# Performance work log

Measured on AMD Instinct MI355X. Metric: run time of the kernel, lower is better.

The kernel has to match this reference:

```python
import jax, jax.numpy as jnp
import numpy as np

N_NODES = 100000
N_EDGES = 1600000
N_FEAT = 128
HIDDEN = 128
OUT = 1
NUM_GRAPHS = 2048


def setup_inputs() -> dict:
    key = jax.random.key(0)
    ks = jax.random.split(key, 8)
    x = jax.random.normal(ks[0], (N_NODES, N_FEAT), dtype=jnp.float32)
    edge_index = jax.random.randint(ks[1], (2, N_EDGES), 0, N_NODES, dtype=jnp.int64)
    batch = jnp.sort(jax.random.randint(ks[2], (N_NODES,), 0, NUM_GRAPHS, dtype=jnp.int64))
    s = 1.0 / np.sqrt(N_FEAT)
    W1 = jax.random.normal(ks[3], (N_FEAT, HIDDEN), dtype=jnp.float32) * s
    b1 = jnp.zeros((HIDDEN,), dtype=jnp.float32)
    W2 = jax.random.normal(ks[4], (HIDDEN, HIDDEN), dtype=jnp.float32) * s
    b2 = jnp.zeros((HIDDEN,), dtype=jnp.float32)
    Wlin = jax.random.normal(ks[5], (HIDDEN, OUT), dtype=jnp.float32) * s
    blin = jnp.zeros((OUT,), dtype=jnp.float32)
    return {"x": x, "edge_index": edge_index, "batch": batch,
            "W1": W1, "b1": b1, "W2": W2, "b2": b2, "Wlin": Wlin, "blin": blin}


def gcn_conv(x, W, b, src, dst, n_nodes):
    # PyG GCNConv: x' = D^{-1/2} (A + I) D^{-1/2} (X W) + b, deg includes self-loop
    xw = x @ W  # [N, H]
    deg = jax.ops.segment_sum(jnp.ones(src.shape[0], xw.dtype), dst, num_segments=n_nodes) + 1.0
    dinv = jax.lax.rsqrt(deg)
    norm = dinv[src] * dinv[dst]  # [E]
    agg = jax.ops.segment_sum(xw[src] * norm[:, None], dst, num_segments=n_nodes)
    # self-loop contribution: norm = deg^{-1}
    return agg + xw * (1.0 / deg)[:, None] + b


def global_mean_pool(x, batch, num_graphs):
    sums = jax.ops.segment_sum(x, batch, num_segments=num_graphs)
    cnts = jax.ops.segment_sum(jnp.ones(x.shape[0], x.dtype), batch, num_segments=num_graphs)
    return sums / jnp.maximum(cnts, 1.0)[:, None]


def reference(x, edge_index, batch, W1, b1, W2, b2, Wlin, blin):
    src, dst = edge_index[0], edge_index[1]
    n = x.shape[0]
    h = gcn_conv(x, W1, b1, src, dst, n)
    h = jax.nn.relu(h)  # dropout is a no-op in eval mode
    h = gcn_conv(h, W2, b2, src, dst, n)
    g = global_mean_pool(h, batch, NUM_GRAPHS)  # [G, H]
    return g @ Wlin + blin
```

## Files before the change

kernel.cpp:

```cpp
#include <hip/hip_runtime.h>

#define N_NODES   100000
#define N_EDGES   1600000
#define NFEAT     128
#define NGRAPHS   2048
#define CBSHIFT   8
#define NCB       ((N_NODES + 255) / 256)
#define P1_EPB    8192
#define GEMM_BLOCKS 782
#define BH_BLOCKS   256
#define DP_BLOCKS 100
#define DP_NPB    ((N_NODES + DP_BLOCKS - 1) / DP_BLOCKS)
#define G1_BLOCKS 2048
#define ZCNT      (NGRAPHS + NCB + 64 + 512 + NCB)

typedef __attribute__((ext_vector_type(8))) short short8;
typedef __attribute__((ext_vector_type(4))) float f32x4;

__device__ __forceinline__ unsigned short f2bf(float f) {
    unsigned int u = __float_as_uint(f);
    u += 0x7FFFu + ((u >> 16) & 1u);
    return (unsigned short)(u >> 16);
}

__device__ __forceinline__ void acc8s(float* acc, uint4 v, float s) {
    acc[0] = fmaf(s, __uint_as_float(v.x << 16), acc[0]);
    acc[1] = fmaf(s, __uint_as_float(v.x & 0xFFFF0000u), acc[1]);
    acc[2] = fmaf(s, __uint_as_float(v.y << 16), acc[2]);
    acc[3] = fmaf(s, __uint_as_float(v.y & 0xFFFF0000u), acc[3]);
    acc[4] = fmaf(s, __uint_as_float(v.z << 16), acc[4]);
    acc[5] = fmaf(s, __uint_as_float(v.z & 0xFFFF0000u), acc[5]);
    acc[6] = fmaf(s, __uint_as_float(v.w << 16), acc[6]);
    acc[7] = fmaf(s, __uint_as_float(v.w & 0xFFFF0000u), acc[7]);
}

__global__ __launch_bounds__(256) void k_misc(const float* __restrict__ W1,
                                              unsigned short* __restrict__ WT1,
                                              const float* __restrict__ W2,
                                              const float* __restrict__ Wlin,
                                              const float* __restrict__ b2,
                                              const float* __restrict__ blin,
                                              float* __restrict__ w2l,
                                              int* __restrict__ zeros) {
    const int blk = blockIdx.x;
    const int t = threadIdx.x;
    if (blk < 16) {
        int base = blk * 1024 + t * 4;
        #pragma unroll
        for (int q = 0; q < 4; ++q) {
            int i = base + q;
            int n = i >> 7, k = i & 127;
            WT1[i] = f2bf(W1[k * 128 + n]);
        }
    } else if (blk == 16) {
        __shared__ float s[256];
        int i = t >> 1, half = t & 1;
        float ps = 0.f;
        for (int j = half * 64; j < half * 64 + 64; ++j)
            ps += W2[i * 128 + j] * Wlin[j];
        s[t] = ps;
        __syncthreads();
        if (!half) w2l[i] = s[t] + s[t + 1];
        __syncthreads();
        float pc = (t < 128) ? b2[t] * Wlin[t] : 0.f;
        s[t] = pc;
        __syncthreads();
        for (int off = 128; off > 0; off >>= 1) {
            if (t < off) s[t] += s[t + off];
            __syncthreads();
        }
        if (t == 0) w2l[128] = s[0] + blin[0];
    } else {
        int i = (blk - 17) * 256 + t;
        if (i < ZCNT) zeros[i] = 0;
    }
}

__global__ __launch_bounds__(256) void k_gemm_bhist(const float* __restrict__ X,
                                                    const unsigned short* __restrict__ WT,
                                                    unsigned short* __restrict__ C,
                                                    const int* __restrict__ dst,
                                                    int* __restrict__ bcount) {
    if (blockIdx.x >= GEMM_BLOCKS) {
        __shared__ int h[NCB];
        for (int i = threadIdx.x; i < NCB; i += 256) h[i] = 0;
        __syncthreads();
        int b = blockIdx.x - GEMM_BLOCKS;
        int stride = BH_BLOCKS * 256;
        for (int e = b * 256 + threadIdx.x; e < N_EDGES; e += stride)
            atomicAdd(&h[dst[e] >> CBSHIFT], 1);
        __syncthreads();
        for (int i = threadIdx.x; i < NCB; i += 256) {
            int v = h[i];
            if (v) atomicAdd(&bcount[i], v);
        }
        return;
    }
    const int tid  = threadIdx.x;
    const int R0   = blockIdx.x * 128;
    const int wv   = tid >> 6;
    const int lane = tid & 63;
    const int m16  = lane & 15;
    const int quad = lane >> 4;
    const int r0 = R0 + wv * 32 + m16;
    const int r1 = r0 + 16;
    const bool ok0 = r0 < N_NODES, ok1 = r1 < N_NODES;

    f32x4 acc[2][8] = {};
    #pragma unroll
    for (int ks = 0; ks < 4; ++ks) {
        const int k0 = ks * 32 + quad * 8;
        short8 a0 = {}, a1 = {};
        if (ok0) {
            float4 f0 = *(const float4*)(X + (size_t)r0 * NFEAT + k0);
            float4 f1 = *(const float4*)(X + (size_t)r0 * NFEAT + k0 + 4);
            a0[0] = (short)f2bf(f0.x); a0[1] = (short)f2bf(f0.y);
            a0[2] = (short)f2bf(f0.z); a0[3] = (short)f2bf(f0.w);
            a0[4] = (short)f2bf(f1.x); a0[5] = (short)f2bf(f1.y);
            a0[6] = (short)f2bf(f1.z); a0[7] = (short)f2bf(f1.w);
        }
        if (ok1) {
            float4 f0 = *(const float4*)(X + (size_t)r1 * NFEAT + k0);
            float4 f1 = *(const float4*)(X + (size_t)r1 * NFEAT + k0 + 4);
            a1[0] = (short)f2bf(f0.x); a1[1] = (short)f2bf(f0.y);
            a1[2] = (short)f2bf(f0.z); a1[3] = (short)f2bf(f0.w);
            a1[4] = (short)f2bf(f1.x); a1[5] = (short)f2bf(f1.y);
            a1[6] = (short)f2bf(f1.z); a1[7] = (short)f2bf(f1.w);
        }
        #pragma unroll
        for (int ct = 0; ct < 8; ++ct) {
            short8 bb = *(const short8*)(WT + (ct * 16 + m16) * 128 + k0);
            acc[0][ct] = __builtin_amdgcn_mfma_f32_16x16x32_bf16(a0, bb, acc[0][ct], 0, 0, 0);
            acc[1][ct] = __builtin_amdgcn_mfma_f32_16x16x32_bf16(a1, bb, acc[1][ct], 0, 0, 0);
        }
    }
    #pragma unroll
    for (int t2 = 0; t2 < 2; ++t2) {
        int rbase = R0 + wv * 32 + t2 * 16 + quad * 4;
        #pragma unroll
        for (int reg = 0; reg < 4; ++reg) {
            int gr = rbase + reg;
            if (gr < N_NODES) {
                #pragma unroll
                for (int ct = 0; ct < 8; ++ct)
                    C[(size_t)gr * NFEAT + ct * 16 + m16] = f2bf(acc[t2][ct][reg]);
            }
        }
    }
}

__global__ __launch_bounds__(256) void k_p1(const int* __restrict__ src,
                                            const int* __restrict__ dst,
                                            const int* __restrict__ bcount,
                                            int* __restrict__ bstart,
                                            int* __restrict__ alloc,
                                            unsigned int* __restrict__ pairs) {
    __shared__ int hist[NCB], base[NCB], cur[NCB], bst[NCB], s[256];
    const int t = threadIdx.x;
    for (int i = t; i < NCB; i += 256) { hist[i] = 0; cur[i] = 0; }
    int v0 = (2 * t < NCB) ? bcount[2 * t] : 0;
    int v1 = (2 * t + 1 < NCB) ? bcount[2 * t + 1] : 0;
    int local = v0 + v1;
    s[t] = local;
    __syncthreads();
    for (int off = 1; off < 256; off <<= 1) {
        int x = (t >= off) ? s[t - off] : 0;
        __syncthreads();
        s[t] += x;
        __syncthreads();
    }
    int excl = s[t] - local;
    if (2 * t < NCB)     bst[2 * t] = excl;
    if (2 * t + 1 < NCB) bst[2 * t + 1] = excl + v0;
    if (blockIdx.x == 0) {
        if (2 * t < NCB)     bstart[2 * t] = excl;
        if (2 * t + 1 < NCB) bstart[2 * t + 1] = excl + v0;
        if (t == 255) bstart[NCB] = s[255];
    }
    __syncthreads();
    const int e0 = blockIdx.x * P1_EPB;
    const int e1 = min(e0 + P1_EPB, N_EDGES);
    for (int e = e0 + t; e < e1; e += 256)
        atomicAdd(&hist[dst[e] >> CBSHIFT], 1);
    __syncthreads();
    const int off0 = (blockIdx.x * 89) % NCB;
    for (int k = t; k < NCB; k += 256) {
        int i = k + off0;
        if (i >= NCB) i -= NCB;
        int c = hist[i];
        base[i] = c ? (bst[i] + atomicAdd(&alloc[i], c)) : 0;
    }
    __syncthreads();
    for (int e = e0 + t; e < e1; e += 256) {
        int d = dst[e];
        int b = d >> CBSHIFT;
        int r = atomicAdd(&cur[b], 1);
        pairs[base[b] + r] = (unsigned int)src[e] | ((unsigned int)(d & 255) << 17);
    }
}

__global__ __launch_bounds__(256) void k_p2(const unsigned int* __restrict__ pairs,
                                            const int* __restrict__ bstart,
                                            int* __restrict__ csr_src,
                                            int* __restrict__ row_start,
                                            int* __restrict__ indeg,
                                            float* __restrict__ dinv,
                                            int* __restrict__ dcount) {
    __shared__ int hist[256], sst[256], cur[256], s[256], dh[64];
    const int b = blockIdx.x;
    const int t = threadIdx.x;
    const int beg = bstart[b];
    const int end = bstart[b + 1];
    hist[t] = 0; cur[t] = 0;
    if (t < 64) dh[t] = 0;
    __syncthreads();
    for (int i = beg + t; i < end; i += 256)
        atomicAdd(&hist[pairs[i] >> 17], 1);
    __syncthreads();
    int v = hist[t];
    s[t] = v;
    __syncthreads();
    for (int off = 1; off < 256; off <<= 1) {
        int x = (t >= off) ? s[t - off] : 0;
        __syncthreads();
        s[t] += x;
        __syncthreads();
    }
    sst[t] = s[t] - v;
    __syncthreads();
    {
        int node = (b << CBSHIFT) + t;
        if (node < N_NODES) {
            row_start[node] = beg + sst[t];
            indeg[node] = v;
            dinv[node] = rsqrtf((float)v + 1.0f);
            atomicAdd(&dh[63 - min(v, 63)], 1);
        }
    }
    for (int i = beg + t; i < end; i += 256) {
        unsigned int pv = pairs[i];
        int dl = pv >> 17;
        int r = atomicAdd(&cur[dl], 1);
        csr_src[beg + sst[dl] + r] = (int)(pv & 0x1FFFFu);
    }
    __syncthreads();
    if (t < 64 && dh[t]) atomicAdd(&dcount[((b & 7) << 6) + t], dh[t]);
}

__global__ __launch_bounds__(256) void k_dperm(const int* __restrict__ indeg,
                                               const int* __restrict__ dcount,
                                               int* __restrict__ dalloc,
                                               int* __restrict__ perm) {
    __shared__ int h[64], base[64], cur[64], s[64];
    const int t = threadIdx.x;
    int v = 0;
    if (t < 64) {
        h[t] = 0; cur[t] = 0;
        #pragma unroll
        for (int sh = 0; sh < 8; ++sh) v += dcount[(sh << 6) + t];
        s[t] = v;
    }
    __syncthreads();
    for (int off = 1; off < 64; off <<= 1) {
        int x = (t >= off && t < 64) ? s[t - off] : 0;
        __syncthreads();
        if (t < 64) s[t] += x;
        __syncthreads();
    }
    int myst = (t < 64) ? s[t] - v : 0;
    const int i0 = blockIdx.x * DP_NPB;
    const int i1 = min(i0 + DP_NPB, N_NODES);
    for (int i = i0 + t; i < i1; i += 256)
        atomicAdd(&h[63 - min(indeg[i], 63)], 1);
    __syncthreads();
    if (t < 64) {
        int c = h[t];
        base[t] = c ? (myst + atomicAdd(&dalloc[t], c)) : 0;
    }
    __syncthreads();
    for (int i = i0 + t; i < i1; i += 256) {
        int bin = 63 - min(indeg[i], 63);
        int r = atomicAdd(&cur[bin], 1);
        perm[base[bin] + r] = i;
    }
}

__global__ __launch_bounds__(256) void k_gather1(const unsigned short* __restrict__ xwb,
                                                 const int* __restrict__ csr_src,
                                                 const int* __restrict__ row_start,
                                                 const int* __restrict__ indeg,
                                                 const float* __restrict__ dinv,
                                                 const float* __restrict__ b,
                                                 const float* __restrict__ w2l,
                                                 const int* __restrict__ perm,
                                                 float* __restrict__ z) {
    const int lane  = threadIdx.x & 63;
    const int p     = lane & 15;
    const int gbase = lane & 48;
    const int ngroups = G1_BLOCKS * 16;
    int gid = blockIdx.x * 16 + (threadIdx.x >> 4);
    const uint4* tab = (const uint4*)xwb;
    float4 b0 = *(const float4*)(b + p * 8);
    float4 b1 = *(const float4*)(b + p * 8 + 4);
    float4 w0 = *(const float4*)(w2l + p * 8);
    float4 w1 = *(const float4*)(w2l + p * 8 + 4);

    for (int nidx = gid; nidx < N_NODES; nidx += ngroups) {
        int node = perm[nidx];
        const int beg = row_start[node];
        const int cnt = indeg[node];
        float dvn = dinv[node];
        float acc[8] = {};
        acc8s(acc, tab[(size_t)node * 16 + p], dvn);
        int j = 0;
        #pragma unroll 1
        for (; j + 8 <= cnt; j += 8) {
            int   my   = csr_src[beg + j + (p & 7)];
            float mydv = dinv[my];
            uint4 v[8];
            #pragma unroll
            for (int q = 0; q < 8; ++q) {
                int idx = __shfl(my, gbase + q);
                v[q] = tab[(size_t)idx * 16 + p];
            }
            #pragma unroll
            for (int q = 0; q < 8; ++q) {
                float sv = __shfl(mydv, gbase + q);
                acc8s(acc, v[q], sv);
            }
        }
        #pragma unroll 1
        for (; j < cnt; ++j) {
            int idx = csr_src[beg + j];
            float sv = dinv[idx];
            acc8s(acc, tab[(size_t)idx * 16 + p], sv);
        }
        float s = fmaxf(acc[0] * dvn + b0.x, 0.f) * w0.x
                + fmaxf(acc[1] * dvn + b0.y, 0.f) * w0.y
                + fmaxf(acc[2] * dvn + b0.z, 0.f) * w0.z
                + fmaxf(acc[3] * dvn + b0.w, 0.f) * w0.w
                + fmaxf(acc[4] * dvn + b1.x, 0.f) * w1.x
                + fmaxf(acc[5] * dvn + b1.y, 0.f) * w1.y
                + fmaxf(acc[6] * dvn + b1.z, 0.f) * w1.z
                + fmaxf(acc[7] * dvn + b1.w, 0.f) * w1.w;
        s += __shfl_xor(s, 1);
        s += __shfl_xor(s, 2);
        s += __shfl_xor(s, 4);
        s += __shfl_xor(s, 8);
        if (p == 0) z[node] = s * dvn;
    }
}

__global__ __launch_bounds__(256) void k_gather2s(const float* __restrict__ z,
                                                  const int* __restrict__ csr_src,
                                                  const int* __restrict__ row_start,
                                                  const int* __restrict__ indeg,
                                                  const float* __restrict__ dinv,
                                                  const int* __restrict__ perm,
                                                  const int* __restrict__ batch,
                                                  float* __restrict__ gsum) {
    int nidx = blockIdx.x * blockDim.x + threadIdx.x;
    if (nidx >= N_NODES) return;
    int node = perm[nidx];
    const int beg = row_start[node];
    const int cnt = indeg[node];
    float a = z[node];
    int j = 0;
    #pragma unroll 1
    for (; j + 4 <= cnt; j += 4) {
        int i0 = csr_src[beg + j + 0];
        int i1 = csr_src[beg + j + 1];
        int i2 = csr_src[beg + j + 2];
        int i3 = csr_src[beg + j + 3];
        a += z[i0] + z[i1] + z[i2] + z[i3];
    }
    #pragma unroll 1
    for (; j < cnt; ++j)
        a += z[csr_src[beg + j]];
    atomicAdd(&gsum[batch[node]], a * dinv[node]);
}

__global__ void k_final(const float* __restrict__ gsum, const int* __restrict__ batch,
                        const float* __restrict__ c2, float* __restrict__ out) {
    int g = blockIdx.x * blockDim.x + threadIdx.x;
    if (g >= NGRAPHS) return;
    int lo = 0, hi = N_NODES;
    while (lo < hi) { int m = (lo + hi) >> 1; if (batch[m] < g) lo = m + 1; else hi = m; }
    int lb = lo;
    lo = 0; hi = N_NODES;
    int g1 = g + 1;
    while (lo < hi) { int m = (lo + hi) >> 1; if (batch[m] < g1) lo = m + 1; else hi = m; }
    float cnt = (float)(lo - lb);
    out[g] = gsum[g] / fmaxf(cnt, 1.0f) + c2[0];
}

extern "C" void kernel_launch(void* const* d_in, const int* in_sizes, int n_in,
                              void* d_out, int out_size, void* d_ws, size_t ws_size,
                              hipStream_t stream) {
    const float* x    = (const float*)d_in[0];
    const int*   ei   = (const int*)d_in[1];
    const int*   bat  = (const int*)d_in[2];
    const float* W1   = (const float*)d_in[3];
    const float* b1   = (const float*)d_in[4];
    const float* W2   = (const float*)d_in[5];
    const float* b2   = (const float*)d_in[6];
    const float* Wlin = (const float*)d_in[7];
    const float* blin = (const float*)d_in[8];
    float* out = (float*)d_out;

    const int* src = ei;
    const int* dst = ei + N_EDGES;

    const size_t NF = (size_t)N_NODES * NFEAT;
    unsigned short* bufA = (unsigned short*)d_ws;
    float* z       = (float*)(bufA + NF);
    float* dinv    = z + N_NODES;
    int* row_start = (int*)(dinv + N_NODES);
    int* indeg     = row_start + N_NODES;
    int* perm      = indeg + N_NODES;
    int* bstart    = perm + N_NODES;
    float* gsum    = (float*)(bstart + NCB + 1);
    int* alloc     = (int*)(gsum + NGRAPHS);
    int* dalloc    = alloc + NCB;
    int* dcount    = dalloc + 64;
    int* bcount    = dcount + 512;
    unsigned short* WT1 = (unsigned short*)(bcount + NCB);
    float* w2l     = (float*)(WT1 + 128 * 128);
    unsigned int* pairs = (unsigned int*)(w2l + 132);
    int* csr_src   = (int*)(pairs + N_EDGES);

    const int BS = 256;
    int p1_blocks   = (N_EDGES + P1_EPB - 1) / P1_EPB;
    int node_blocks = (N_NODES + BS - 1) / BS;
    int misc_blocks = 17 + (ZCNT + BS - 1) / BS;

    k_misc<<<misc_blocks, BS, 0, stream>>>(W1, WT1, W2, Wlin, b2, blin, w2l, (int*)gsum);
    k_gemm_bhist<<<GEMM_BLOCKS + BH_BLOCKS, BS, 0, stream>>>(x, WT1, bufA, dst, bcount);

    k_p1<<<p1_blocks, BS, 0, stream>>>(src, dst, bcount, bstart, alloc, pairs);
    k_p2<<<NCB, BS, 0, stream>>>(pairs, bstart, csr_src, row_start, indeg, dinv, dcount);
    k_dperm<<<DP_BLOCKS, BS, 0, stream>>>(indeg, dcount, dalloc, perm);

    k_gather1<<<G1_BLOCKS, BS, 0, stream>>>(bufA, csr_src, row_start, indeg, dinv, b1, w2l,
                                            perm, z);

    k_gather2s<<<node_blocks, BS, 0, stream>>>(z, csr_src, row_start, indeg, dinv, perm,
                                               bat, gsum);

    k_final<<<(NGRAPHS + BS - 1) / BS, BS, 0, stream>>>(gsum, bat, w2l + 128, out);
}
```

Before: 284.7 us.

## Fuse misc prep into GEMM kernel and fold final pooling into gather2

Removes the separate misc kernel. Each GEMM block now transposes and converts W1 to bf16 itself in shared memory, and the W2·Wlin and per-graph inverse-count work runs as extra blocks of the GEMM launch. The final kernel is folded into gather2 with a last-block-done counter, and zeroing now uses hipMemsetAsync. This cuts two kernel launches and their serialization gaps, at the cost of each GEMM block redoing the W1 conversion and a global atomic counter plus fence in gather2.

```diff
diff --git a/kernel.cpp b/kernel.cpp
--- a/kernel.cpp
+++ b/kernel.cpp
@@ -9,10 +9,12 @@
 #define P1_EPB    8192
 #define GEMM_BLOCKS 782
 #define BH_BLOCKS   256
+#define GC_BLOCKS   8
 #define DP_BLOCKS 100
 #define DP_NPB    ((N_NODES + DP_BLOCKS - 1) / DP_BLOCKS)
 #define G1_BLOCKS 2048
-#define ZCNT      (NGRAPHS + NCB + 64 + 512 + NCB)
+#define G2_BLOCKS ((N_NODES + 255) / 256)
+#define ZCNT      (NGRAPHS + NCB + 64 + 512 + NCB + 1)
 
 typedef __attribute__((ext_vector_type(8))) short short8;
 typedef __attribute__((ext_vector_type(4))) float f32x4;
@@ -34,72 +36,87 @@
     acc[7] = fmaf(s, __uint_as_float(v.w & 0xFFFF0000u), acc[7]);
 }
 
-__global__ __launch_bounds__(256) void k_misc(const float* __restrict__ W1,
-                                              unsigned short* __restrict__ WT1,
-                                              const float* __restrict__ W2,
-                                              const float* __restrict__ Wlin,
-                                              const float* __restrict__ b2,
-                                              const float* __restrict__ blin,
-                                              float* __restrict__ w2l,
-                                              int* __restrict__ zeros) {
+__global__ __launch_bounds__(256) void k_gemm_bhist(const float* __restrict__ X,
+                                                    const float* __restrict__ W1,
+                                                    unsigned short* __restrict__ C,
+                                                    const int* __restrict__ dst,
+                                                    int* __restrict__ bcount,
+                                                    const int* __restrict__ batch,
+                                                    float* __restrict__ invc,
+                                                    const float* __restrict__ W2,
+                                                    const float* __restrict__ Wlin,
+                                                    const float* __restrict__ b2,
+                                                    const float* __restrict__ blin,
+                                                    float* __restrict__ w2l) {
+    __shared__ unsigned short Ws[128][136];
     const int blk = blockIdx.x;
     const int t = threadIdx.x;
-    if (blk < 16) {
-        int base = blk * 1024 + t * 4;
-        #pragma unroll
-        for (int q = 0; q < 4; ++q) {
-            int i = base + q;
-            int n = i >> 7, k = i & 127;
-            WT1[i] = f2bf(W1[k * 128 + n]);
-        }
-    } else if (blk == 16) {
-        __shared__ float s[256];
+
+    if (blk >= GEMM_BLOCKS + BH_BLOCKS + GC_BLOCKS) {
+        __shared__ float fs[256];
         int i = t >> 1, half = t & 1;
         float ps = 0.f;
         for (int j = half * 64; j < half * 64 + 64; ++j)
             ps += W2[i * 128 + j] * Wlin[j];
-        s[t] = ps;
-        __syncthreads();
-        if (!half) w2l[i] = s[t] + s[t + 1];
+        fs[t] = ps;
+        __syncthreads();
+        if (!half) w2l[i] = fs[t] + fs[t + 1];
         __syncthreads();
         float pc = (t < 128) ? b2[t] * Wlin[t] : 0.f;
-        s[t] = pc;
+        fs[t] = pc;
         __syncthreads();
         for (int off = 128; off > 0; off >>= 1) {
-            if (t < off) s[t] += s[t + off];
+            if (t < off) fs[t] += fs[t + off];
             __syncthreads();
         }
-        if (t == 0) w2l[128] = s[0] + blin[0];
-    } else {
-        int i = (blk - 17) * 256 + t;
-        if (i < ZCNT) zeros[i] = 0;
-    }
-}
-
-__global__ __launch_bounds__(256) void k_gemm_bhist(const float* __restrict__ X,
-                                                    const unsigned short* __restrict__ WT,
-                                                    unsigned short* __restrict__ C,
-                                                    const int* __restrict__ dst,
-                                                    int* __restrict__ bcount) {
-    if (blockIdx.x >= GEMM_BLOCKS) {
-        __shared__ int h[NCB];
-        for (int i = threadIdx.x; i < NCB; i += 256) h[i] = 0;
-        __syncthreads();
-        int b = blockIdx.x - GEMM_BLOCKS;
+        if (t == 0) w2l[128] = fs[0] + blin[0];
+        return;
+    }
+    if (blk >= GEMM_BLOCKS + BH_BLOCKS) {
+        int g = (blk - GEMM_BLOCKS - BH_BLOCKS) * 256 + t;
+        if (g < NGRAPHS) {
+            int lo = 0, hi = N_NODES;
+            while (lo < hi) { int m = (lo + hi) >> 1; if (batch[m] < g) lo = m + 1; else hi = m; }
+            int lb = lo;
+            lo = 0; hi = N_NODES;
+            int g1 = g + 1;
+            while (lo < hi) { int m = (lo + hi) >> 1; if (batch[m] < g1) lo = m + 1; else hi = m; }
+            invc[g] = 1.0f / fmaxf((float)(lo - lb), 1.0f);
+        }
+        return;
+    }
+    if (blk >= GEMM_BLOCKS) {
+        int* h = (int*)&Ws[0][0];
+        for (int i = t; i < NCB; i += 256) h[i] = 0;
+        __syncthreads();
+        int b = blk - GEMM_BLOCKS;
         int stride = BH_BLOCKS * 256;
-        for (int e = b * 256 + threadIdx.x; e < N_EDGES; e += stride)
+        for (int e = b * 256 + t; e < N_EDGES; e += stride)
             atomicAdd(&h[dst[e] >> CBSHIFT], 1);
         __syncthreads();
-        for (int i = threadIdx.x; i < NCB; i += 256) {
+        for (int i = t; i < NCB; i += 256) {
             int v = h[i];
             if (v) atomicAdd(&bcount[i], v);
         }
         return;
     }
-    const int tid  = threadIdx.x;
-    const int R0   = blockIdx.x * 128;
-    const int wv   = tid >> 6;
-    const int lane = tid & 63;
+    {
+        int base = t * 4;
+        #pragma unroll
+        for (int it = 0; it < 16; ++it) {
+            int i = it * 1024 + base;
+            int k = i >> 7, n = i & 127;
+            float4 f = *(const float4*)(W1 + i);
+            Ws[n + 0][k] = f2bf(f.x);
+            Ws[n + 1][k] = f2bf(f.y);
+            Ws[n + 2][k] = f2bf(f.z);
+            Ws[n + 3][k] = f2bf(f.w);
+        }
+    }
+    __syncthreads();
+    const int R0   = blk * 128;
+    const int wv   = t >> 6;
+    const int lane = t & 63;
     const int m16  = lane & 15;
     const int quad = lane >> 4;
     const int r0 = R0 + wv * 32 + m16;
@@ -129,7 +146,7 @@
         }
         #pragma unroll
         for (int ct = 0; ct < 8; ++ct) {
-            short8 bb = *(const short8*)(WT + (ct * 16 + m16) * 128 + k0);
+            short8 bb = *(const short8*)(&Ws[ct * 16 + m16][k0]);
             acc[0][ct] = __builtin_amdgcn_mfma_f32_16x16x32_bf16(a0, bb, acc[0][ct], 0, 0, 0);
             acc[1][ct] = __builtin_amdgcn_mfma_f32_16x16x32_bf16(a1, bb, acc[1][ct], 0, 0, 0);
         }
@@ -358,40 +375,44 @@
                                                   const float* __restrict__ dinv,
                                                   const int* __restrict__ perm,
                                                   const int* __restrict__ batch,
-                                                  float* __restrict__ gsum) {
+                                                  float* __restrict__ gsum,
+                                                  const float* __restrict__ invc,
+                                                  const float* __restrict__ w2l,
+                                                  int* __restrict__ done,
+                                                  float* __restrict__ out) {
     int nidx = blockIdx.x * blockDim.x + threadIdx.x;
-    if (nidx >= N_NODES) return;
-    int node = perm[nidx];
-    const int beg = row_start[node];
-    const int cnt = indeg[node];
-    float a = z[node];
-    int j = 0;
-    #pragma unroll 1
-    for (; j + 4 <= cnt; j += 4) {
-        int i0 = csr_src[beg + j + 0];
-        int i1 = csr_src[beg + j + 1];
-        int i2 = csr_src[beg + j + 2];
-        int i3 = csr_src[beg + j + 3];
-        a += z[i0] + z[i1] + z[i2] + z[i3];
-    }
-    #pragma unroll 1
-    for (; j < cnt; ++j)
-        a += z[csr_src[beg + j]];
-    atomicAdd(&gsum[batch[node]], a * dinv[node]);
-}
-
-__global__ void k_final(const float* __restrict__ gsum, const int* __restrict__ batch,
-                        const float* __restrict__ c2, float* __restrict__ out) {
-    int g = blockIdx.x * blockDim.x + threadIdx.x;
-    if (g >= NGRAPHS) return;
-    int lo = 0, hi = N_NODES;
-    while (lo < hi) { int m = (lo + hi) >> 1; if (batch[m] < g) lo = m + 1; else hi = m; }
-    int lb = lo;
-    lo = 0; hi = N_NODES;
-    int g1 = g + 1;
-    while (lo < hi) { int m = (lo + hi) >> 1; if (batch[m] < g1) lo = m + 1; else hi = m; }
-    float cnt = (float)(lo - lb);
-    out[g] = gsum[g] / fmaxf(cnt, 1.0f) + c2[0];
+    if (nidx < N_NODES) {
+        int node = perm[nidx];
+        const int beg = row_start[node];
+        const int cnt = indeg[node];
+        float a = z[node];
+        int j = 0;
+        #pragma unroll 1
+        for (; j + 4 <= cnt; j += 4) {
+            int i0 = csr_src[beg + j + 0];
+            int i1 = csr_src[beg + j + 1];
+            int i2 = csr_src[beg + j + 2];
+            int i3 = csr_src[beg + j + 3];
+            a += z[i0] + z[i1] + z[i2] + z[i3];
+        }
+        #pragma unroll 1
+        for (; j < cnt; ++j)
+            a += z[csr_src[beg + j]];
+        atomicAdd(&gsum[batch[node]], a * dinv[node]);
+    }
+    __threadfence();
+    __syncthreads();
+    __shared__ int lastBlk;
+    if (threadIdx.x == 0)
+        lastBlk = (atomicAdd(done, 1) == (int)gridDim.x - 1) ? 1 : 0;
+    __syncthreads();
+    if (lastBlk) {
+        float c2 = w2l[128];
+        for (int g = threadIdx.x; g < NGRAPHS; g += 256) {
+            float v = atomicAdd(&gsum[g], 0.0f);
+            out[g] = v * invc[g] + c2;
+        }
+    }
 }
 
 extern "C" void kernel_launch(void* const* d_in, const int* in_sizes, int n_in,
@@ -424,18 +445,19 @@
     int* dalloc    = alloc + NCB;
     int* dcount    = dalloc + 64;
     int* bcount    = dcount + 512;
-    unsigned short* WT1 = (unsigned short*)(bcount + NCB);
-    float* w2l     = (float*)(WT1 + 128 * 128);
-    unsigned int* pairs = (unsigned int*)(w2l + 132);
+    int* done      = bcount + NCB;
+    float* w2l     = (float*)(done + 1);
+    float* invc    = w2l + 132;
+    unsigned int* pairs = (unsigned int*)(invc + NGRAPHS);
     int* csr_src   = (int*)(pairs + N_EDGES);
 
     const int BS = 256;
-    int p1_blocks   = (N_EDGES + P1_EPB - 1) / P1_EPB;
-    int node_blocks = (N_NODES + BS - 1) / BS;
-    int misc_blocks = 17 + (ZCNT + BS - 1) / BS;
-
-    k_misc<<<misc_blocks, BS, 0, stream>>>(W1, WT1, W2, Wlin, b2, blin, w2l, (int*)gsum);
-    k_gemm_bhist<<<GEMM_BLOCKS + BH_BLOCKS, BS, 0, stream>>>(x, WT1, bufA, dst, bcount);
+    int p1_blocks = (N_EDGES + P1_EPB - 1) / P1_EPB;
+
+    hipMemsetAsync(gsum, 0, ZCNT * sizeof(int), stream);
+
+    k_gemm_bhist<<<GEMM_BLOCKS + BH_BLOCKS + GC_BLOCKS + 1, BS, 0, stream>>>(
+        x, W1, bufA, dst, bcount, bat, invc, W2, Wlin, b2, blin, w2l);
 
     k_p1<<<p1_blocks, BS, 0, stream>>>(src, dst, bcount, bstart, alloc, pairs);
     k_p2<<<NCB, BS, 0, stream>>>(pairs, bstart, csr_src, row_start, indeg, dinv, dcount);
@@ -444,8 +466,6 @@
     k_gather1<<<G1_BLOCKS, BS, 0, stream>>>(bufA, csr_src, row_start, indeg, dinv, b1, w2l,
                                             perm, z);
 
-    k_gather2s<<<node_blocks, BS, 0, stream>>>(z, csr_src, row_start, indeg, dinv, perm,
-                                               bat, gsum);
-
-    k_final<<<(NGRAPHS + BS - 1) / BS, BS, 0, stream>>>(gsum, bat, w2l + 128, out);
-}
+    k_gather2s<<<G2_BLOCKS, BS, 0, stream>>>(z, csr_src, row_start, indeg, dinv, perm,
+                                             bat, gsum, invc, w2l, done, out);
+}
```

Result: slower. 303.6 us (+6.6%).
